# Kernel tuning notes

Hardware: AMD Instinct MI355X
Metric: run time of the kernel (lower is better)

## Reference

```python
import jax, jax.numpy as jnp
import numpy as np

# UKF constants (Merwe scaled sigma points)
ALPHA, BETA, KAPPA = 1.0, 2.0, 0.0
JITTER = 1e-4
S_DIM, C_DIM, M_DIM, H_DIM = 8, 2, 4, 32


def setup_inputs() -> dict:
    B, T = 1024, 256
    key = jax.random.key(0)
    ks = jax.random.split(key, 11)
    inp = {
        "X0": 0.1 * jax.random.normal(ks[0], (B, S_DIM), dtype=jnp.float32),
        "u": jax.random.normal(ks[1], (B, T, C_DIM), dtype=jnp.float32),
        "y": jax.random.normal(ks[2], (B, T, M_DIM), dtype=jnp.float32),
        # learned process model f(x,u) = x + tanh([x;u] W1 + b1) W2 + b2
        "W1": 0.1 * jax.random.normal(ks[3], (S_DIM + C_DIM, H_DIM), dtype=jnp.float32),
        "b1": jnp.zeros((H_DIM,), dtype=jnp.float32),
        "W2": 0.1 * jax.random.normal(ks[4], (H_DIM, S_DIM), dtype=jnp.float32),
        "b2": jnp.zeros((S_DIM,), dtype=jnp.float32),
        # linear measurement model h(x) = Hm x
        "Hm": 0.3 * jax.random.normal(ks[5], (M_DIM, S_DIM), dtype=jnp.float32),
        # learned diagonal noise / initial covariance (softplus parameterized)
        "lq": -3.0 + 0.1 * jax.random.normal(ks[6], (S_DIM,), dtype=jnp.float32),
        "lr": -2.0 + 0.1 * jax.random.normal(ks[7], (M_DIM,), dtype=jnp.float32),
        "lp0": -1.0 + 0.1 * jax.random.normal(ks[8], (S_DIM,), dtype=jnp.float32),
    }
    return inp


def reference(X0, u, y, W1, b1, W2, b2, Hm, lq, lr, lp0):
    B, n = X0.shape
    T = u.shape[1]
    lam = ALPHA ** 2 * (n + KAPPA) - n
    c = n + lam
    Wm = jnp.concatenate([jnp.array([lam / c], dtype=X0.dtype),
                          jnp.full((2 * n,), 0.5 / c, dtype=X0.dtype)])
    Wc = Wm.at[0].add(1.0 - ALPHA ** 2 + BETA)
    I = jnp.eye(n, dtype=X0.dtype)

    Q = jnp.diag(jax.nn.softplus(lq))            # [n,n] process noise
    R = jnp.diag(jax.nn.softplus(lr))            # [m,m] measurement noise
    P0 = jnp.broadcast_to(jnp.diag(jax.nn.softplus(lp0)), (B, n, n))  # P0(X0)

    def f(pts, u_t):  # pts [B,2n+1,n], u_t [B,C]
        uu = jnp.broadcast_to(u_t[:, None, :], pts.shape[:2] + (u_t.shape[-1],))
        z = jnp.concatenate([pts, uu], axis=-1)
        return pts + jnp.tanh(z @ W1 + b1) @ W2 + b2

    def step(carry, inp_t):
        x, P = carry            # x [B,n], P [B,n,n]
        u_t, y_t = inp_t        # u at i-1, y at i
        # sigma points via Cholesky of scaled covariance
        L = jnp.linalg.cholesky(c * P + JITTER * I)
        offs = jnp.swapaxes(L, -1, -2)  # [B,n,n]: row i = i-th column of L
        pts = jnp.concatenate([x[:, None], x[:, None] + offs, x[:, None] - offs], axis=1)  # [B,2n+1,n]
        # predict
        pts_f = f(pts, u_t)
        x_pred = jnp.einsum('s,bsn->bn', Wm, pts_f)
        dx = pts_f - x_pred[:, None]
        P_pred = jnp.einsum('s,bsn,bsm->bnm', Wc, dx, dx) + Q
        P_pred = 0.5 * (P_pred + jnp.swapaxes(P_pred, -1, -2)) + JITTER * I
        # measurement update (linear h reused on propagated sigma points)
        y_pts = pts_f @ Hm.T
        y_pred = jnp.einsum('s,bsm->bm', Wm, y_pts)
        dy = y_pts - y_pred[:, None]
        Sy = jnp.einsum('s,bsi,bsj->bij', Wc, dy, dy) + R
        Sy = 0.5 * (Sy + jnp.swapaxes(Sy, -1, -2))
        Pxy = jnp.einsum('s,bsn,bsm->bnm', Wc, dx, dy)
        # K = Pxy Sy^{-1} via solve on Sy (SPD)
        K = jnp.swapaxes(jnp.linalg.solve(Sy, jnp.swapaxes(Pxy, -1, -2)), -1, -2)
        x_new = x_pred + jnp.einsum('bnm,bm->bn', K, y_t - y_pred)
        P_new = P_pred - K @ Sy @ jnp.swapaxes(K, -1, -2)
        P_new = 0.5 * (P_new + jnp.swapaxes(P_new, -1, -2)) + JITTER * I
        q_e = 0.5 * jnp.linalg.slogdet(P_pred)[1]  # [B]
        r_e = 0.5 * jnp.linalg.slogdet(Sy)[1]      # [B]
        return (x_new, P_new), (x_new, P_new, q_e, r_e)

    # steps i = 1..T-1 use u[:, i-1] and y[:, i]
    u_seq = jnp.swapaxes(u[:, :T - 1], 0, 1)  # [T-1,B,C]
    y_seq = jnp.swapaxes(y[:, 1:], 0, 1)      # [T-1,B,M]
    _, (Xs, Ps, qs, rs) = jax.lax.scan(step, (X0, P0), (u_seq, y_seq))

    X = jnp.concatenate([X0[:, None], jnp.swapaxes(Xs, 0, 1)], axis=1)        # [B,T,n]
    P = jnp.concatenate([P0[:, None], jnp.swapaxes(Ps, 0, 1)], axis=1)        # [B,T,n,n]
    zcol = jnp.zeros((X0.shape[0], 1), dtype=X0.dtype)
    q_entr = jnp.concatenate([zcol, jnp.swapaxes(qs, 0, 1)], axis=1)          # [B,T]
    r_entr = jnp.concatenate([zcol, jnp.swapaxes(rs, 0, 1)], axis=1)          # [B,T]
    return X, P, q_entr, r_entr
```

## Files before the change

kernel.cpp:

```cpp
#include <hip/hip_runtime.h>
#include <math.h>

#define B_LEN 1024
#define T_LEN 256
#define HST 36
#define TS 20

__device__ __forceinline__ float fast_rcp(float x) { return __builtin_amdgcn_rcpf(x); }
__device__ __forceinline__ float fast_rsq(float x) { return __builtin_amdgcn_rsqf(x); }
__device__ __forceinline__ float lane_bcast(float v, int l) {
    return __int_as_float(__builtin_amdgcn_readlane(__float_as_int(v), l));
}
__device__ __forceinline__ float fast_tanh(float x) {
    float e = __expf(2.0f * x);
    return 1.0f - 2.0f * fast_rcp(e + 1.0f);
}
__device__ __forceinline__ float softplus_f(float x) {
    return (x > 20.0f) ? x : log1pf(expf(x));
}
__device__ __forceinline__ float wdot17(const float* __restrict__ a,
                                        const float* __restrict__ b) {
    float full = 0.0f;
    #pragma unroll
    for (int c = 0; c < 4; ++c) {
        const float4 av = *(const float4*)&a[c * 4];
        const float4 bv = *(const float4*)&b[c * 4];
        full += av.x * bv.x + av.y * bv.y + av.z * bv.z + av.w * bv.w;
    }
    full += a[16] * b[16];
    return 0.0625f * full + 1.9375f * a[0] * b[0];
}

__global__ __launch_bounds__(128, 2)
void ukf_kernel(const float* __restrict__ X0, const float* __restrict__ U,
                const float* __restrict__ Y,  const float* __restrict__ W1,
                const float* __restrict__ B1, const float* __restrict__ W2,
                const float* __restrict__ B2, const float* __restrict__ HM,
                const float* __restrict__ LQ, const float* __restrict__ LR,
                const float* __restrict__ LP0, float* __restrict__ out)
{
    const int tid  = threadIdx.x;
    const int wid  = tid >> 6;
    const int lane = tid & 63;
    const int b    = blockIdx.x;
    const int k8   = lane & 7;
    const int g8   = lane >> 3;
    const int i8   = g8;
    const int j8   = k8;
    const int h32  = lane & 31;
    const int p2   = lane >> 5;
    const int m4   = lane & 3;
    const int sy   = lane >> 2;

    __shared__ __align__(16) float u_sh[T_LEN * 2];
    __shared__ __align__(16) float y_sh[T_LEN * 4];
    __shared__ __align__(16) float pts_sh[17 * 8];
    __shared__ __align__(16) float hid_sh[17 * HST];
    __shared__ __align__(16) float pf_sh[17 * 8];
    __shared__ __align__(16) float dxT_sh[8 * TS];
    __shared__ __align__(16) float ypT_sh[4 * TS];
    __shared__ __align__(16) float xp_sh[8];
    __shared__ __align__(16) float ypred_sh[4];
    __shared__ __align__(16) float Sy_sh[16];
    __shared__ __align__(16) float Si_sh[16];
    __shared__ __align__(16) float Pxy_sh[32];
    __shared__ __align__(16) float Pp_sh[64];

    for (int k = tid; k < T_LEN * 2; k += 128) u_sh[k] = U[(size_t)b * (T_LEN * 2) + k];
    for (int k = tid; k < T_LEN * 4; k += 128) y_sh[k] = Y[(size_t)b * (T_LEN * 4) + k];

    float w1r[10];
    #pragma unroll
    for (int d = 0; d < 10; ++d) w1r[d] = W1[d * 32 + h32];
    const float b1r = B1[h32];
    float w2r[32];
    #pragma unroll
    for (int h = 0; h < 32; ++h) w2r[h] = W2[h * 8 + k8];
    const float b2r = B2[k8];
    float hmr[8];
    #pragma unroll
    for (int d = 0; d < 8; ++d) hmr[d] = HM[m4 * 8 + d];

    const float qdiag = softplus_f(LQ[i8]);
    const float rdiag = softplus_f(LR[m4]);

    const size_t Xbase = (size_t)b * T_LEN * 8;
    const size_t Pbase = (size_t)B_LEN * T_LEN * 8  + (size_t)b * T_LEN * 64;
    const size_t qbase = (size_t)B_LEN * T_LEN * 72 + (size_t)b * T_LEN;
    const size_t rbase = (size_t)B_LEN * T_LEN * 73 + (size_t)b * T_LEN;

    float xn[8], Pc[8];
    {
        const float4 xa = *(const float4*)&X0[b * 8];
        const float4 xb = *(const float4*)&X0[b * 8 + 4];
        xn[0] = xa.x; xn[1] = xa.y; xn[2] = xa.z; xn[3] = xa.w;
        xn[4] = xb.x; xn[5] = xb.y; xn[6] = xb.z; xn[7] = xb.w;
        const float p0k = softplus_f(LP0[k8]);
        #pragma unroll
        for (int i = 0; i < 8; ++i) Pc[i] = (i == k8) ? p0k : 0.0f;
    }
    if (wid == 0) {
        out[Pbase + lane] = Pc[g8];
        if (lane == 0) {
            *(float4*)&out[Xbase]     = make_float4(xn[0], xn[1], xn[2], xn[3]);
            *(float4*)&out[Xbase + 4] = make_float4(xn[4], xn[5], xn[6], xn[7]);
            out[qbase] = 0.0f; out[rbase] = 0.0f;
        }
    }

    for (int t = 1; t < T_LEN; ++t) {
        if (wid == 0) {
            float a[8];
            #pragma unroll
            for (int i = 0; i < 8; ++i) a[i] = 8.0f * Pc[i] + ((i == k8) ? 1e-4f : 0.0f);
            #pragma unroll
            for (int j = 0; j < 8; ++j) {
                const float dj = lane_bcast(a[j], j);
                const float rv = fast_rsq(dj);
                const float sc = (k8 == j) ? rv : 1.0f;
                const float tc = (k8 > j) ? a[j] * (rv * rv) : 0.0f;
                float u[8];
                #pragma unroll
                for (int i = j + 1; i < 8; ++i) u[i] = lane_bcast(a[i], j);
                #pragma unroll
                for (int i = j + 1; i < 8; ++i) a[i] = sc * a[i] - tc * u[i];
                a[j] = (k8 == j) ? dj * rv : a[j];
            }
            float Lc[8];
            #pragma unroll
            for (int i = 0; i < 8; ++i) Lc[i] = (i >= k8) ? a[i] : 0.0f;
            if (g8 == 0) {
                *(float4*)&pts_sh[(1 + k8) * 8] =
                    make_float4(xn[0] + Lc[0], xn[1] + Lc[1], xn[2] + Lc[2], xn[3] + Lc[3]);
                *(float4*)&pts_sh[(1 + k8) * 8 + 4] =
                    make_float4(xn[4] + Lc[4], xn[5] + Lc[5], xn[6] + Lc[6], xn[7] + Lc[7]);
            } else if (g8 == 1) {
                *(float4*)&pts_sh[(9 + k8) * 8] =
                    make_float4(xn[0] - Lc[0], xn[1] - Lc[1], xn[2] - Lc[2], xn[3] - Lc[3]);
                *(float4*)&pts_sh[(9 + k8) * 8 + 4] =
                    make_float4(xn[4] - Lc[4], xn[5] - Lc[5], xn[6] - Lc[6], xn[7] - Lc[7]);
            } else if (g8 == 2 && k8 == 0) {
                *(float4*)&pts_sh[0] = make_float4(xn[0], xn[1], xn[2], xn[3]);
                *(float4*)&pts_sh[4] = make_float4(xn[4], xn[5], xn[6], xn[7]);
            }
        }
        __syncthreads();

        {
            const float u0 = u_sh[(t - 1) * 2 + 0];
            const float u1 = u_sh[(t - 1) * 2 + 1];
            const float ub = b1r + u0 * w1r[8] + u1 * w1r[9];
            if (wid == 0) {
                #pragma unroll
                for (int p = 0; p < 4; ++p) {
                    const int s = 2 * p + p2;
                    const float4 pa = *(const float4*)&pts_sh[s * 8];
                    const float4 pb = *(const float4*)&pts_sh[s * 8 + 4];
                    float acc = ub
                        + pa.x * w1r[0] + pa.y * w1r[1] + pa.z * w1r[2] + pa.w * w1r[3]
                        + pb.x * w1r[4] + pb.y * w1r[5] + pb.z * w1r[6] + pb.w * w1r[7];
                    hid_sh[s * HST + h32] = fast_tanh(acc);
                }
            } else {
                #pragma unroll
                for (int p = 0; p < 4; ++p) {
                    const int s = 8 + 2 * p + p2;
                    const float4 pa = *(const float4*)&pts_sh[s * 8];
                    const float4 pb = *(const float4*)&pts_sh[s * 8 + 4];
                    float acc = ub
                        + pa.x * w1r[0] + pa.y * w1r[1] + pa.z * w1r[2] + pa.w * w1r[3]
                        + pb.x * w1r[4] + pb.y * w1r[5] + pb.z * w1r[6] + pb.w * w1r[7];
                    hid_sh[s * HST + h32] = fast_tanh(acc);
                }
                if (p2 == 0) {
                    const float4 pa = *(const float4*)&pts_sh[16 * 8];
                    const float4 pb = *(const float4*)&pts_sh[16 * 8 + 4];
                    float acc = ub
                        + pa.x * w1r[0] + pa.y * w1r[1] + pa.z * w1r[2] + pa.w * w1r[3]
                        + pb.x * w1r[4] + pb.y * w1r[5] + pb.z * w1r[6] + pb.w * w1r[7];
                    hid_sh[16 * HST + h32] = fast_tanh(acc);
                }
            }
            const int srow = (wid == 0) ? g8 : (8 + g8);
            float acc = b2r;
            #pragma unroll
            for (int h = 0; h < 32; h += 4) {
                const float4 hv = *(const float4*)&hid_sh[srow * HST + h];
                acc += hv.x * w2r[h] + hv.y * w2r[h + 1] + hv.z * w2r[h + 2] + hv.w * w2r[h + 3];
            }
            pf_sh[srow * 8 + k8] = pts_sh[srow * 8 + k8] + acc;
            if (wid == 1 && lane < 8) {
                float a16 = b2r;
                #pragma unroll
                for (int h = 0; h < 32; h += 4) {
                    const float4 hv = *(const float4*)&hid_sh[16 * HST + h];
                    a16 += hv.x * w2r[h] + hv.y * w2r[h + 1] + hv.z * w2r[h + 2] + hv.w * w2r[h + 3];
                }
                pf_sh[16 * 8 + lane] = pts_sh[16 * 8 + lane] + a16;
            }
        }
        __syncthreads();

        if (wid == 0) {
            const float v0   = pf_sh[i8 * 8 + j8];
            const float v1   = pf_sh[(8 + i8) * 8 + j8];
            const float pf16 = (i8 == 0) ? pf_sh[16 * 8 + j8] : 0.0f;
            float part = ((i8 == 0) ? pf16 : v0) + v1;
            part += __shfl_xor(part, 8);
            part += __shfl_xor(part, 16);
            part += __shfl_xor(part, 32);
            const float xp = part * 0.0625f;
            if (i8 == 0) xp_sh[j8] = xp;
            dxT_sh[j8 * TS + i8]       = v0 - xp;
            dxT_sh[j8 * TS + 8 + i8]   = v1 - xp;
            if (i8 == 0) dxT_sh[j8 * TS + 16] = pf16 - xp;
        } else {
            float yv0, yv16 = 0.0f;
            {
                const float4 pa = *(const float4*)&pf_sh[sy * 8];
                const float4 pb = *(const float4*)&pf_sh[sy * 8 + 4];
                yv0 = pa.x * hmr[0] + pa.y * hmr[1] + pa.z * hmr[2] + pa.w * hmr[3]
                    + pb.x * hmr[4] + pb.y * hmr[5] + pb.z * hmr[6] + pb.w * hmr[7];
            }
            if (sy == 0) {
                const float4 pa = *(const float4*)&pf_sh[16 * 8];
                const float4 pb = *(const float4*)&pf_sh[16 * 8 + 4];
                yv16 = pa.x * hmr[0] + pa.y * hmr[1] + pa.z * hmr[2] + pa.w * hmr[3]
                     + pb.x * hmr[4] + pb.y * hmr[5] + pb.z * hmr[6] + pb.w * hmr[7];
            }
            float py = (sy == 0) ? yv16 : yv0;
            py += __shfl_xor(py, 4);
            py += __shfl_xor(py, 8);
            py += __shfl_xor(py, 16);
            py += __shfl_xor(py, 32);
            const float ypred = py * 0.0625f;
            if (lane < 4) ypred_sh[lane] = ypred;
            ypT_sh[m4 * TS + sy] = yv0 - ypred;
            if (sy == 0) ypT_sh[m4 * TS + 16] = yv16 - ypred;
        }
        __syncthreads();

        float Ppc[8];
        if (wid == 0) {
            const float Ppred = wdot17(&dxT_sh[i8 * TS], &dxT_sh[j8 * TS])
                              + ((i8 == j8) ? (qdiag + 1e-4f) : 0.0f);
            Pp_sh[lane] = Ppred;
            const float4 pa = *(const float4*)&Pp_sh[k8 * 8];
            const float4 pb = *(const float4*)&Pp_sh[k8 * 8 + 4];
            Ppc[0]=pa.x; Ppc[1]=pa.y; Ppc[2]=pa.z; Ppc[3]=pa.w;
            Ppc[4]=pb.x; Ppc[5]=pb.y; Ppc[6]=pb.z; Ppc[7]=pb.w;
        } else {
            const int r2 = (lane < 32) ? sy : (sy & 3);
            const float* pa2 = (lane < 32) ? &dxT_sh[r2 * TS] : &ypT_sh[r2 * TS];
            float v2 = wdot17(pa2, &ypT_sh[m4 * TS]);
            v2 += ((lane >= 32) && (r2 == m4)) ? rdiag : 0.0f;
            if (lane < 32)      Pxy_sh[lane] = v2;
            else if (lane < 48) Sy_sh[r2 * 4 + m4] = v2;
            float cof;
            {
                const int i4 = sy & 3;
                const int j4 = m4;
                const int r0 = (i4 == 0) ? 1 : 0;
                const int r1 = (i4 <= 1) ? 2 : 1;
                const int rr = (i4 <= 2) ? 3 : 2;
                const int c0 = (j4 == 0) ? 1 : 0;
                const int c1 = (j4 <= 1) ? 2 : 1;
                const int cc = (j4 <= 2) ? 3 : 2;
                const float m00 = Sy_sh[r0 * 4 + c0], m01 = Sy_sh[r0 * 4 + c1], m02 = Sy_sh[r0 * 4 + cc];
                const float m10 = Sy_sh[r1 * 4 + c0], m11 = Sy_sh[r1 * 4 + c1], m12 = Sy_sh[r1 * 4 + cc];
                const float m20 = Sy_sh[rr * 4 + c0], m21 = Sy_sh[rr * 4 + c1], m22 = Sy_sh[rr * 4 + cc];
                const float d3 = m00 * (m11 * m22 - m12 * m21)
                               - m01 * (m10 * m22 - m12 * m20)
                               + m02 * (m10 * m21 - m11 * m20);
                cof = (((i4 + j4) & 1) ? -d3 : d3);
            }
            const float c0b = lane_bcast(cof, 0);
            const float c1b = lane_bcast(cof, 1);
            const float c2b = lane_bcast(cof, 2);
            const float c3b = lane_bcast(cof, 3);
            const float4 sy0 = *(const float4*)&Sy_sh[0];
            const float det = sy0.x * c0b + sy0.y * c1b + sy0.z * c2b + sy0.w * c3b;
            if (lane == 0) out[rbase + t] = 0.5f * __logf(det);
            const float rdet = fast_rcp(det);
            if (lane < 16) Si_sh[lane] = cof * rdet;
        }
        __syncthreads();

        if (wid == 0) {
            float Si[16];
            {
                const float4 a0 = *(const float4*)&Si_sh[0];
                const float4 a1 = *(const float4*)&Si_sh[4];
                const float4 a2 = *(const float4*)&Si_sh[8];
                const float4 a3 = *(const float4*)&Si_sh[12];
                Si[0]=a0.x;  Si[1]=a0.y;  Si[2]=a0.z;  Si[3]=a0.w;
                Si[4]=a1.x;  Si[5]=a1.y;  Si[6]=a1.z;  Si[7]=a1.w;
                Si[8]=a2.x;  Si[9]=a2.y;  Si[10]=a2.z; Si[11]=a2.w;
                Si[12]=a3.x; Si[13]=a3.y; Si[14]=a3.z; Si[15]=a3.w;
            }
            const float4 pr = *(const float4*)&Pxy_sh[k8 * 4];
            float kk[4];
            #pragma unroll
            for (int aa = 0; aa < 4; ++aa)
                kk[aa] = pr.x * Si[0 * 4 + aa] + pr.y * Si[1 * 4 + aa]
                       + pr.z * Si[2 * 4 + aa] + pr.w * Si[3 * 4 + aa];
            float Pr[32];
            {
                const float4 q0 = *(const float4*)&Pxy_sh[0];
                const float4 q1 = *(const float4*)&Pxy_sh[4];
                const float4 q2 = *(const float4*)&Pxy_sh[8];
                const float4 q3 = *(const float4*)&Pxy_sh[12];
                const float4 q4 = *(const float4*)&Pxy_sh[16];
                const float4 q5 = *(const float4*)&Pxy_sh[20];
                const float4 q6 = *(const float4*)&Pxy_sh[24];
                const float4 q7 = *(const float4*)&Pxy_sh[28];
                Pr[0]=q0.x;  Pr[1]=q0.y;  Pr[2]=q0.z;  Pr[3]=q0.w;
                Pr[4]=q1.x;  Pr[5]=q1.y;  Pr[6]=q1.z;  Pr[7]=q1.w;
                Pr[8]=q2.x;  Pr[9]=q2.y;  Pr[10]=q2.z; Pr[11]=q2.w;
                Pr[12]=q3.x; Pr[13]=q3.y; Pr[14]=q3.z; Pr[15]=q3.w;
                Pr[16]=q4.x; Pr[17]=q4.y; Pr[18]=q4.z; Pr[19]=q4.w;
                Pr[20]=q5.x; Pr[21]=q5.y; Pr[22]=q5.z; Pr[23]=q5.w;
                Pr[24]=q6.x; Pr[25]=q6.y; Pr[26]=q6.z; Pr[27]=q6.w;
                Pr[28]=q7.x; Pr[29]=q7.y; Pr[30]=q7.z; Pr[31]=q7.w;
            }
            #pragma unroll
            for (int i = 0; i < 8; ++i) {
                const float m = kk[0] * Pr[i * 4 + 0] + kk[1] * Pr[i * 4 + 1]
                              + kk[2] * Pr[i * 4 + 2] + kk[3] * Pr[i * 4 + 3];
                Pc[i] = Ppc[i] - m + ((i == k8) ? 1e-4f : 0.0f);
            }
            const float4 yt = *(const float4*)&y_sh[t * 4];
            const float4 yp = *(const float4*)&ypred_sh[0];
            const float in0 = yt.x - yp.x, in1 = yt.y - yp.y;
            const float in2 = yt.z - yp.z, in3 = yt.w - yp.w;
            const float xo = xp_sh[k8]
                           + kk[0] * in0 + kk[1] * in1 + kk[2] * in2 + kk[3] * in3;
            #pragma unroll
            for (int i = 0; i < 8; ++i) xn[i] = lane_bcast(xo, i);
            out[Pbase + (size_t)t * 64 + lane] = Pc[g8];
            if (lane == 0) {
                *(float4*)&out[Xbase + (size_t)t * 8]     = make_float4(xn[0], xn[1], xn[2], xn[3]);
                *(float4*)&out[Xbase + (size_t)t * 8 + 4] = make_float4(xn[4], xn[5], xn[6], xn[7]);
            }
        } else {
            float aq[8];
            {
                const float4 pa = *(const float4*)&Pp_sh[k8 * 8];
                const float4 pb = *(const float4*)&Pp_sh[k8 * 8 + 4];
                aq[0]=pa.x; aq[1]=pa.y; aq[2]=pa.z; aq[3]=pa.w;
                aq[4]=pb.x; aq[5]=pb.y; aq[6]=pb.z; aq[7]=pb.w;
            }
            float qe = 0.0f;
            #pragma unroll
            for (int j = 0; j < 8; ++j) {
                const float dj  = lane_bcast(aq[j], j);
                qe += __logf(dj);
                const float rv2 = fast_rcp(dj);
                const float tq  = (k8 > j) ? aq[j] * rv2 : 0.0f;
                float u[8];
                #pragma unroll
                for (int i = j + 1; i < 8; ++i) u[i] = lane_bcast(aq[i], j);
                #pragma unroll
                for (int i = j + 1; i < 8; ++i) aq[i] = fmaf(-tq, u[i], aq[i]);
            }
            if (lane == 0) out[qbase + t] = 0.5f * qe;
        }
    }
}

extern "C" void kernel_launch(void* const* d_in, const int* in_sizes, int n_in,
                              void* d_out, int out_size, void* d_ws, size_t ws_size,
                              hipStream_t stream) {
    (void)in_sizes; (void)n_in; (void)out_size; (void)d_ws; (void)ws_size;
    const float* X0 = (const float*)d_in[0];
    const float* U  = (const float*)d_in[1];
    const float* Y  = (const float*)d_in[2];
    const float* W1 = (const float*)d_in[3];
    const float* B1 = (const float*)d_in[4];
    const float* W2 = (const float*)d_in[5];
    const float* B2 = (const float*)d_in[6];
    const float* HM = (const float*)d_in[7];
    const float* LQ = (const float*)d_in[8];
    const float* LR = (const float*)d_in[9];
    const float* LP0 = (const float*)d_in[10];
    float* out = (float*)d_out;
    ukf_kernel<<<dim3(B_LEN), dim3(128), 0, stream>>>(X0, U, Y, W1, B1, W2, B2,
                                                      HM, LQ, LR, LP0, out);
}
```

Before: 797.6 us.

## Split per-block UKF work across four wavefronts instead of two

Raises the block size from 128 to 256 threads so each batch element is handled by four wavefronts. The sigma-point MLP (hidden tanh layer and output projection) is redistributed so each wave handles about four sigma points rather than eight. The Pxy and Sy covariance reductions move onto separate waves 2 and 3 so they run in parallel. The aim is a shorter per-timestep critical path in this latency-bound recurrence. In exchange, every block barrier now synchronises four waves, and the tighter launch bound may limit registers enough to cause spills of the register-cached weights.

```diff
diff --git a/kernel.cpp b/kernel.cpp
--- a/kernel.cpp
+++ b/kernel.cpp
@@ -31,7 +31,7 @@
     return 0.0625f * full + 1.9375f * a[0] * b[0];
 }
 
-__global__ __launch_bounds__(128, 2)
+__global__ __launch_bounds__(256, 4)
 void ukf_kernel(const float* __restrict__ X0, const float* __restrict__ U,
                 const float* __restrict__ Y,  const float* __restrict__ W1,
                 const float* __restrict__ B1, const float* __restrict__ W2,
@@ -66,8 +66,8 @@
     __shared__ __align__(16) float Pxy_sh[32];
     __shared__ __align__(16) float Pp_sh[64];
 
-    for (int k = tid; k < T_LEN * 2; k += 128) u_sh[k] = U[(size_t)b * (T_LEN * 2) + k];
-    for (int k = tid; k < T_LEN * 4; k += 128) y_sh[k] = Y[(size_t)b * (T_LEN * 4) + k];
+    for (int k = tid; k < T_LEN * 2; k += 256) u_sh[k] = U[(size_t)b * (T_LEN * 2) + k];
+    for (int k = tid; k < T_LEN * 4; k += 256) y_sh[k] = Y[(size_t)b * (T_LEN * 4) + k];
 
     float w1r[10];
     #pragma unroll
@@ -150,53 +150,41 @@
             const float u0 = u_sh[(t - 1) * 2 + 0];
             const float u1 = u_sh[(t - 1) * 2 + 1];
             const float ub = b1r + u0 * w1r[8] + u1 * w1r[9];
-            if (wid == 0) {
-                #pragma unroll
-                for (int p = 0; p < 4; ++p) {
-                    const int s = 2 * p + p2;
-                    const float4 pa = *(const float4*)&pts_sh[s * 8];
-                    const float4 pb = *(const float4*)&pts_sh[s * 8 + 4];
-                    float acc = ub
-                        + pa.x * w1r[0] + pa.y * w1r[1] + pa.z * w1r[2] + pa.w * w1r[3]
-                        + pb.x * w1r[4] + pb.y * w1r[5] + pb.z * w1r[6] + pb.w * w1r[7];
-                    hid_sh[s * HST + h32] = fast_tanh(acc);
+            #pragma unroll
+            for (int p = 0; p < 2; ++p) {
+                const int s = 4 * wid + 2 * p + p2;
+                const float4 pa = *(const float4*)&pts_sh[s * 8];
+                const float4 pb = *(const float4*)&pts_sh[s * 8 + 4];
+                float acc = ub
+                    + pa.x * w1r[0] + pa.y * w1r[1] + pa.z * w1r[2] + pa.w * w1r[3]
+                    + pb.x * w1r[4] + pb.y * w1r[5] + pb.z * w1r[6] + pb.w * w1r[7];
+                hid_sh[s * HST + h32] = fast_tanh(acc);
+            }
+            if (wid == 3 && p2 == 0) {
+                const float4 pa = *(const float4*)&pts_sh[16 * 8];
+                const float4 pb = *(const float4*)&pts_sh[16 * 8 + 4];
+                float acc = ub
+                    + pa.x * w1r[0] + pa.y * w1r[1] + pa.z * w1r[2] + pa.w * w1r[3]
+                    + pb.x * w1r[4] + pb.y * w1r[5] + pb.z * w1r[6] + pb.w * w1r[7];
+                hid_sh[16 * HST + h32] = fast_tanh(acc);
+            }
+            if (g8 < 4) {
+                const int srow = 4 * wid + g8;
+                float acc = b2r;
+                #pragma unroll
+                for (int h = 0; h < 32; h += 4) {
+                    const float4 hv = *(const float4*)&hid_sh[srow * HST + h];
+                    acc += hv.x * w2r[h] + hv.y * w2r[h + 1] + hv.z * w2r[h + 2] + hv.w * w2r[h + 3];
                 }
-            } else {
-                #pragma unroll
-                for (int p = 0; p < 4; ++p) {
-                    const int s = 8 + 2 * p + p2;
-                    const float4 pa = *(const float4*)&pts_sh[s * 8];
-                    const float4 pb = *(const float4*)&pts_sh[s * 8 + 4];
-                    float acc = ub
-                        + pa.x * w1r[0] + pa.y * w1r[1] + pa.z * w1r[2] + pa.w * w1r[3]
-                        + pb.x * w1r[4] + pb.y * w1r[5] + pb.z * w1r[6] + pb.w * w1r[7];
-                    hid_sh[s * HST + h32] = fast_tanh(acc);
-                }
-                if (p2 == 0) {
-                    const float4 pa = *(const float4*)&pts_sh[16 * 8];
-                    const float4 pb = *(const float4*)&pts_sh[16 * 8 + 4];
-                    float acc = ub
-                        + pa.x * w1r[0] + pa.y * w1r[1] + pa.z * w1r[2] + pa.w * w1r[3]
-                        + pb.x * w1r[4] + pb.y * w1r[5] + pb.z * w1r[6] + pb.w * w1r[7];
-                    hid_sh[16 * HST + h32] = fast_tanh(acc);
-                }
-            }
-            const int srow = (wid == 0) ? g8 : (8 + g8);
-            float acc = b2r;
-            #pragma unroll
-            for (int h = 0; h < 32; h += 4) {
-                const float4 hv = *(const float4*)&hid_sh[srow * HST + h];
-                acc += hv.x * w2r[h] + hv.y * w2r[h + 1] + hv.z * w2r[h + 2] + hv.w * w2r[h + 3];
-            }
-            pf_sh[srow * 8 + k8] = pts_sh[srow * 8 + k8] + acc;
-            if (wid == 1 && lane < 8) {
+                pf_sh[srow * 8 + k8] = pts_sh[srow * 8 + k8] + acc;
+            } else if (wid == 3 && g8 == 4) {
                 float a16 = b2r;
                 #pragma unroll
                 for (int h = 0; h < 32; h += 4) {
                     const float4 hv = *(const float4*)&hid_sh[16 * HST + h];
                     a16 += hv.x * w2r[h] + hv.y * w2r[h + 1] + hv.z * w2r[h + 2] + hv.w * w2r[h + 3];
                 }
-                pf_sh[16 * 8 + lane] = pts_sh[16 * 8 + lane] + a16;
+                pf_sh[16 * 8 + k8] = pts_sh[16 * 8 + k8] + a16;
             }
         }
         __syncthreads();
@@ -214,7 +202,7 @@
             dxT_sh[j8 * TS + i8]       = v0 - xp;
             dxT_sh[j8 * TS + 8 + i8]   = v1 - xp;
             if (i8 == 0) dxT_sh[j8 * TS + 16] = pf16 - xp;
-        } else {
+        } else if (wid == 1) {
             float yv0, yv16 = 0.0f;
             {
                 const float4 pa = *(const float4*)&pf_sh[sy * 8];
@@ -249,13 +237,13 @@
             const float4 pb = *(const float4*)&Pp_sh[k8 * 8 + 4];
             Ppc[0]=pa.x; Ppc[1]=pa.y; Ppc[2]=pa.z; Ppc[3]=pa.w;
             Ppc[4]=pb.x; Ppc[5]=pb.y; Ppc[6]=pb.z; Ppc[7]=pb.w;
-        } else {
-            const int r2 = (lane < 32) ? sy : (sy & 3);
-            const float* pa2 = (lane < 32) ? &dxT_sh[r2 * TS] : &ypT_sh[r2 * TS];
-            float v2 = wdot17(pa2, &ypT_sh[m4 * TS]);
-            v2 += ((lane >= 32) && (r2 == m4)) ? rdiag : 0.0f;
-            if (lane < 32)      Pxy_sh[lane] = v2;
-            else if (lane < 48) Sy_sh[r2 * 4 + m4] = v2;
+        } else if (wid == 2) {
+            if (lane < 32)
+                Pxy_sh[lane] = wdot17(&dxT_sh[sy * TS], &ypT_sh[m4 * TS]);
+        } else if (wid == 3) {
+            if (lane < 16)
+                Sy_sh[lane] = wdot17(&ypT_sh[sy * TS], &ypT_sh[m4 * TS])
+                            + ((sy == m4) ? rdiag : 0.0f);
             float cof;
             {
                 const int i4 = sy & 3;
@@ -342,7 +330,7 @@
                 *(float4*)&out[Xbase + (size_t)t * 8]     = make_float4(xn[0], xn[1], xn[2], xn[3]);
                 *(float4*)&out[Xbase + (size_t)t * 8 + 4] = make_float4(xn[4], xn[5], xn[6], xn[7]);
             }
-        } else {
+        } else if (wid == 1) {
             float aq[8];
             {
                 const float4 pa = *(const float4*)&Pp_sh[k8 * 8];
@@ -384,6 +372,6 @@
     const float* LR = (const float*)d_in[9];
     const float* LP0 = (const float*)d_in[10];
     float* out = (float*)d_out;
-    ukf_kernel<<<dim3(B_LEN), dim3(128), 0, stream>>>(X0, U, Y, W1, B1, W2, B2,
+    ukf_kernel<<<dim3(B_LEN), dim3(256), 0, stream>>>(X0, U, Y, W1, B1, W2, B2,
                                                       HM, LQ, LR, LP0, out);
 }
```

New measurement: 2.538 ms. 3.18x slower.
